# Performance work log

Measured on AMD Instinct MI355X. Metric: run time of the kernel, lower is better.

## Reference

```python
import jax, jax.numpy as jnp
import numpy as np

NUM_HEADS = 12
LOCAL_WINDOW = 7


def setup_inputs() -> dict:
    key = jax.random.key(0)
    k1, k2, k3 = jax.random.split(key, 3)
    B, N, C = 2, 2048, 768
    x = jax.random.normal(k1, (B, N, C), dtype=jnp.float32)
    w_qkv = jax.random.normal(k2, (3 * C, C), dtype=jnp.float32) * (C ** -0.5)
    w_proj = jax.random.normal(k3, (C, C), dtype=jnp.float32) * (C ** -0.5)
    b_proj = jnp.zeros((C,), dtype=jnp.float32)
    return {"x": x, "w_qkv": w_qkv, "w_proj": w_proj, "b_proj": b_proj}


def reference(x, w_qkv, w_proj, b_proj):
    B, N, C = x.shape
    H = NUM_HEADS
    Dh = C // H
    scale = Dh ** -0.5
    # local-window additive mask: 0 within |i-j|<=w, -inf outside (vectorized)
    idx = jnp.arange(N)
    local_mask = jnp.where(
        jnp.abs(idx[:, None] - idx[None, :]) <= LOCAL_WINDOW, 0.0, -jnp.inf
    ).astype(x.dtype)
    qkv = x @ w_qkv.T
    qkv = qkv.reshape(B, N, 3, H, Dh).transpose(2, 0, 3, 1, 4)
    q, k, v = qkv[0], qkv[1], qkv[2]
    attn = jnp.einsum("bhnd,bhmd->bhnm", q, k) * scale
    attn = attn + local_mask[None, None, :, :]
    attn = jax.nn.softmax(attn, axis=-1)
    out = jnp.einsum("bhnm,bhmd->bhnd", attn, v)
    out = out.transpose(0, 2, 1, 3).reshape(B, N, C)
    return out @ w_proj.T + b_proj
```

## Files before the change

### kernel.cpp

```cpp
#include <hip/hip_runtime.h>
#include <hip/hip_bf16.h>

typedef __bf16 bf16;
typedef bf16 bf16x4 __attribute__((ext_vector_type(4)));
typedef bf16 bf16x8 __attribute__((ext_vector_type(8)));
typedef float floatx4 __attribute__((ext_vector_type(4)));

#define GLOBAL_AS __attribute__((address_space(1)))
#define LDS_AS __attribute__((address_space(3)))

__global__ __launch_bounds__(256)
void cvt3_f32_bf16(const float* __restrict__ s0, const float* __restrict__ s1,
                   const float* __restrict__ s2, bf16* __restrict__ d0,
                   bf16* __restrict__ d1, bf16* __restrict__ d2,
                   int n0, int n1, int n2)
{
    int t = blockIdx.x * blockDim.x + threadIdx.x;
    const float* s; bf16* d; int i;
    if (t < n0)                { s = s0; d = d0; i = t; }
    else if (t < n0 + n1)      { s = s1; d = d1; i = t - n0; }
    else if (t < n0 + n1 + n2) { s = s2; d = d2; i = t - n0 - n1; }
    else return;
    float4 v = ((const float4*)s)[i];
    bf16x4 o = { (bf16)v.x, (bf16)v.y, (bf16)v.z, (bf16)v.w };
    ((bf16x4*)d)[i] = o;
}

template<typename CT, bool AF32, bool WF32, int TM, int M, int N, int K,
         int LDA, int LDC>
__global__ __launch_bounds__(256, 2)
void gemm_bt(const void* __restrict__ Av, const void* __restrict__ Wv,
             CT* __restrict__ C, const float* __restrict__ bias)
{
    constexpr int MI = TM / 32;
    __shared__ __align__(16) bf16 As[TM * 32];
    __shared__ __align__(16) bf16 Bs[128 * 32];

    const int tid  = threadIdx.x;
    const int lane = tid & 63;
    const int wave = tid >> 6;

    const int lin = blockIdx.y * gridDim.x + blockIdx.x;
    const int ch  = gridDim.x >> 3;
    const int xcd = lin & 7;
    const int rr  = lin >> 3;
    const int bx  = xcd * ch + (rr % ch);
    const int by  = rr / ch;

    const int row0 = bx * TM;
    const int col0 = by * 128;

    const int wm = (wave & 1) * (TM / 2);
    const int wn = (wave >> 1) * 64;

    floatx4 acc[MI][4] = {};

    const int fr = lane & 15;
    const int fk = (lane >> 4) * 8;

    const int lr = lane >> 2;
    const int lk = (lane & 3) * 8;

    for (int k0 = 0; k0 < K; k0 += 32) {
        if (AF32) {
            constexpr int NV = TM * 4;
            #pragma unroll
            for (int c = 0; c < NV / 256; ++c) {
                const int idx = tid + c * 256;
                const int r   = idx >> 2;
                const int cb  = (idx & 3) * 8;
                const float4* g = (const float4*)((const float*)Av
                                   + (size_t)(row0 + r) * LDA + k0 + cb);
                float4 g0 = g[0], g1 = g[1];
                bf16x8 va;
                va[0]=(bf16)g0.x; va[1]=(bf16)g0.y; va[2]=(bf16)g0.z; va[3]=(bf16)g0.w;
                va[4]=(bf16)g1.x; va[5]=(bf16)g1.y; va[6]=(bf16)g1.z; va[7]=(bf16)g1.w;
                *(bf16x8*)(As + r * 32 + cb) = va;
            }
        } else {
            constexpr int CAW = TM / 64;
            #pragma unroll
            for (int c = 0; c < CAW; ++c) {
                const int chunk = wave * CAW + c;
                const int r = chunk * 16 + lr;
                const bf16* gA = (const bf16*)Av + (size_t)(row0 + r) * LDA + k0 + lk;
                __builtin_amdgcn_global_load_lds((const GLOBAL_AS void*)gA,
                                                 (LDS_AS void*)(As + chunk * 512),
                                                 16, 0, 0);
            }
        }
        if (WF32) {
            #pragma unroll
            for (int c = 0; c < 2; ++c) {
                const int idx = tid + c * 256;
                const int r   = idx >> 2;
                const int cb  = (idx & 3) * 8;
                const float4* g = (const float4*)((const float*)Wv
                                   + (size_t)(col0 + r) * K + k0 + cb);
                float4 g0 = g[0], g1 = g[1];
                bf16x8 vw;
                vw[0]=(bf16)g0.x; vw[1]=(bf16)g0.y; vw[2]=(bf16)g0.z; vw[3]=(bf16)g0.w;
                vw[4]=(bf16)g1.x; vw[5]=(bf16)g1.y; vw[6]=(bf16)g1.z; vw[7]=(bf16)g1.w;
                *(bf16x8*)(Bs + r * 32 + cb) = vw;
            }
        } else {
            #pragma unroll
            for (int c = 0; c < 2; ++c) {
                const int chunk = wave * 2 + c;
                const int r = chunk * 16 + lr;
                const bf16* gB = (const bf16*)Wv + (size_t)(col0 + r) * K + k0 + lk;
                __builtin_amdgcn_global_load_lds((const GLOBAL_AS void*)gB,
                                                 (LDS_AS void*)(Bs + chunk * 512),
                                                 16, 0, 0);
            }
        }
        __syncthreads();

        bf16x8 af[MI], bfr[4];
        #pragma unroll
        for (int i = 0; i < MI; ++i)
            af[i]  = *(const bf16x8*)(As + (wm + i * 16 + fr) * 32 + fk);
        #pragma unroll
        for (int j = 0; j < 4; ++j)
            bfr[j] = *(const bf16x8*)(Bs + (wn + j * 16 + fr) * 32 + fk);
        #pragma unroll
        for (int i = 0; i < MI; ++i)
            #pragma unroll
            for (int j = 0; j < 4; ++j)
                acc[i][j] = __builtin_amdgcn_mfma_f32_16x16x32_bf16(
                    af[i], bfr[j], acc[i][j], 0, 0, 0);

        __syncthreads();
    }

    const int fc  = lane & 15;
    const int fr4 = (lane >> 4) * 4;
    #pragma unroll
    for (int i = 0; i < MI; ++i) {
        #pragma unroll
        for (int j = 0; j < 4; ++j) {
            const int col = col0 + wn + j * 16 + fc;
            const float b = bias ? bias[col] : 0.0f;
            #pragma unroll
            for (int r = 0; r < 4; ++r) {
                const int row = row0 + wm + i * 16 + fr4 + r;
                C[(size_t)row * LDC + col] = (CT)(acc[i][j][r] + b);
            }
        }
    }
}

__global__ __launch_bounds__(256)
void attn_tile(const bf16* __restrict__ qkv, bf16* __restrict__ aout)
{
    __shared__ __align__(16) bf16 Vt[4][64][40];
    __shared__ __align__(16) bf16 Ps[4][16][40];

    const int w    = threadIdx.x >> 6;
    const int lane = threadIdx.x & 63;
    const int c    = lane & 15;
    const int q    = lane >> 4;
    int bid = blockIdx.x;
    bid = (bid & 7) * 96 + (bid >> 3);
    const int wid  = bid * 4 + w;
    const int it   = wid & 127;
    const int bh   = wid >> 7;
    const int h    = bh % 12;
    const int b    = bh / 12;
    const int I0   = it * 16;
    const int bbase = b * 2048;
    const int j0   = I0 - 7;

    #pragma unroll
    for (int itr = 0; itr < 4; ++itr) {
        int idx = itr * 64 + lane;
        int row = idx >> 3;
        int dc  = (idx & 7) * 8;
        int jc  = j0 + row; jc = jc < 0 ? 0 : (jc > 2047 ? 2047 : jc);
        const bf16* base = qkv + (size_t)(bbase + jc) * 2304 + 1536 + h * 64 + dc;
        bf16x8 vv = *(const bf16x8*)base;
        #pragma unroll
        for (int e = 0; e < 8; ++e) {
            int d    = dc + e;
            int col2 = (row * 2) ^ (((d >> 3) & 3) << 4);
            *(bf16*)((char*)&Vt[w][d][0] + col2) = vv[e];
        }
    }

    const bf16* qrow = qkv + (size_t)(bbase + I0 + c) * 2304 + h * 64;
    bf16x8 aq0 = *(const bf16x8*)(qrow + q * 8);
    bf16x8 aq1 = *(const bf16x8*)(qrow + 32 + q * 8);

    floatx4 st[2] = {};
    #pragma unroll
    for (int t = 0; t < 2; ++t) {
        int jr = j0 + t * 16 + c;
        jr = jr < 0 ? 0 : (jr > 2047 ? 2047 : jr);
        const bf16* krow = qkv + (size_t)(bbase + jr) * 2304 + 768 + h * 64;
        bf16x8 k0 = *(const bf16x8*)(krow + q * 8);
        bf16x8 k1 = *(const bf16x8*)(krow + 32 + q * 8);
        st[t] = __builtin_amdgcn_mfma_f32_16x16x32_bf16(aq0, k0, st[t], 0, 0, 0);
        st[t] = __builtin_amdgcn_mfma_f32_16x16x32_bf16(aq1, k1, st[t], 0, 0, 0);
    }

    float s[2][4];
    #pragma unroll
    for (int t = 0; t < 2; ++t)
        #pragma unroll
        for (int r = 0; r < 4; ++r) {
            int il = q * 4 + r;
            int jl = t * 16 + c;
            int ja = j0 + jl;
            bool valid = (jl >= il) && (jl <= il + 14) && (ja >= 0) && (ja < 2048);
            s[t][r] = valid ? st[t][r] * 0.125f : -1e30f;
        }

    float l[4], p[2][4];
    #pragma unroll
    for (int r = 0; r < 4; ++r) {
        float m2 = fmaxf(s[0][r], s[1][r]);
        #pragma unroll
        for (int mk = 1; mk < 16; mk <<= 1) m2 = fmaxf(m2, __shfl_xor(m2, mk, 64));
        p[0][r] = __expf(s[0][r] - m2);
        p[1][r] = __expf(s[1][r] - m2);
        float l2 = p[0][r] + p[1][r];
        #pragma unroll
        for (int mk = 1; mk < 16; mk <<= 1) l2 += __shfl_xor(l2, mk, 64);
        l[r] = l2;
    }

    #pragma unroll
    for (int r = 0; r < 4; ++r) {
        Ps[w][q * 4 + r][c]      = (bf16)p[0][r];
        Ps[w][q * 4 + r][16 + c] = (bf16)p[1][r];
    }

    bf16x8 ap = *(const bf16x8*)(&Ps[w][c][q * 8]);
    floatx4 ov[4];
    #pragma unroll
    for (int nt = 0; nt < 4; ++nt) {
        int dr = nt * 16 + c;
        int cb = (q * 16) ^ (((dr >> 3) & 3) << 4);
        bf16x8 vf = *(const bf16x8*)((const char*)&Vt[w][dr][0] + cb);
        floatx4 z = {};
        ov[nt] = __builtin_amdgcn_mfma_f32_16x16x32_bf16(ap, vf, z, 0, 0, 0);
    }

    float rl[4];
    #pragma unroll
    for (int r = 0; r < 4; ++r) rl[r] = 1.0f / l[r];
    #pragma unroll
    for (int r = 0; r < 4; ++r) {
        bf16* orow = aout + (size_t)(bbase + I0 + q * 4 + r) * 768 + h * 64;
        #pragma unroll
        for (int nt = 0; nt < 4; ++nt)
            orow[nt * 16 + c] = (bf16)(ov[nt][r] * rl[r]);
    }
}

extern "C" void kernel_launch(void* const* d_in, const int* in_sizes, int n_in,
                              void* d_out, int out_size, void* d_ws, size_t ws_size,
                              hipStream_t stream)
{
    const float* x      = (const float*)d_in[0];
    const float* w_qkv  = (const float*)d_in[1];
    const float* w_proj = (const float*)d_in[2];
    const float* b_proj = (const float*)d_in[3];
    float* out = (float*)d_out;

    bf16* qkv = (bf16*)d_ws;
    const size_t QKV_B  = (size_t)4096 * 2304 * 2;
    const size_t AO_B   = (size_t)4096 * 768 * 2;
    const size_t XB_B   = (size_t)4096 * 768 * 2;
    const size_t WQKV_B = (size_t)2304 * 768 * 2;
    const size_t WPRJ_B = (size_t)768 * 768 * 2;

    if (ws_size >= QKV_B + AO_B + XB_B + WQKV_B + WPRJ_B) {
        bf16* aout = (bf16*)((char*)d_ws + QKV_B);
        bf16* xb   = (bf16*)((char*)aout + AO_B);
        bf16* wqb  = (bf16*)((char*)xb + XB_B);
        bf16* wpb  = (bf16*)((char*)wqb + WQKV_B);

        const int n0 = 4096 * 768 / 4, n1 = 2304 * 768 / 4, n2 = 768 * 768 / 4;
        cvt3_f32_bf16<<<dim3((n0 + n1 + n2) / 256), 256, 0, stream>>>(
            x, w_qkv, w_proj, xb, wqb, wpb, n0, n1, n2);

        gemm_bt<bf16, false, false, 128, 4096, 2304, 768, 768, 2304>
            <<<dim3(32, 18), 256, 0, stream>>>(xb, wqb, qkv, nullptr);

        attn_tile<<<dim3(768), 256, 0, stream>>>(qkv, aout);

        gemm_bt<float, false, false, 64, 4096, 768, 768, 768, 768>
            <<<dim3(64, 6), 256, 0, stream>>>(aout, wpb, out, b_proj);
    } else {
        gemm_bt<bf16, true, true, 128, 4096, 2304, 768, 768, 2304>
            <<<dim3(32, 18), 256, 0, stream>>>(x, w_qkv, qkv, nullptr);

        bf16* aout = (bf16*)((char*)d_ws + QKV_B);
        attn_tile<<<dim3(768), 256, 0, stream>>>(qkv, aout);

        gemm_bt<float, false, true, 64, 4096, 768, 768, 768, 768>
            <<<dim3(64, 6), 256, 0, stream>>>(aout, w_proj, out, b_proj);
    }
}
```

Measured before the change: 121.9 us.

## Use 256x256-tile 8-wave GEMM with direct-to-LDS loads for QKV projection

Adds a new GEMM kernel with 512 threads and 256x256 output tiles. It double-buffers K=64 slices loaded straight into LDS via global_load_lds with XOR swizzling, and splits MFMA work into quadrants with set-priority and barriers. It replaces the older 128-row tile GEMM for the QKV projection only. The goal is more data reuse per block and overlapping loads with compute. In exchange it launches only 144 blocks, fewer than the number of CUs, and uses 128KB of LDS, which limits occupancy.

```diff
diff --git a/kernel.cpp b/kernel.cpp
--- a/kernel.cpp
+++ b/kernel.cpp
@@ -8,6 +8,12 @@
 
 #define GLOBAL_AS __attribute__((address_space(1)))
 #define LDS_AS __attribute__((address_space(3)))
+
+__device__ __forceinline__ void hard_barrier() {
+    asm volatile("" ::: "memory");
+    __builtin_amdgcn_s_barrier();
+    asm volatile("" ::: "memory");
+}
 
 __global__ __launch_bounds__(256)
 void cvt3_f32_bf16(const float* __restrict__ s0, const float* __restrict__ s1,
@@ -26,6 +32,125 @@
     ((bf16x4*)d)[i] = o;
 }
 
+template<typename CT, int M, int N, int K, int LDA, int LDC>
+__global__ __launch_bounds__(512, 2)
+void gemm8p_bt(const bf16* __restrict__ A, const bf16* __restrict__ W,
+               CT* __restrict__ C)
+{
+    constexpr int NT = K / 64;
+    __shared__ __align__(16) bf16 lds[2][2][256 * 64];
+
+    const int tid  = threadIdx.x;
+    const int lane = tid & 63;
+    const int wave = tid >> 6;
+
+    int lin = blockIdx.x;
+    const int chx = gridDim.x >> 3;
+    lin = (lin & 7) * chx + (lin >> 3);
+    const int bx = lin / (N / 256);
+    const int by = lin % (N / 256);
+    const int row0 = bx * 256;
+    const int col0 = by * 256;
+
+    const int wm = (wave & 1) * 128;
+    const int wn = (wave >> 1) * 64;
+
+    const int fr  = lane & 15;
+    const int fks = lane >> 4;
+    const int fr7 = fr & 7;
+
+    const int rl = tid >> 3;
+    const int sl = tid & 7;
+    const int ss = sl ^ (rl & 7);
+
+    floatx4 acc[8][4] = {};
+
+    auto stage = [&](const bf16* G, int ldg, int g0, int k0, bf16* Ld) {
+        #pragma unroll
+        for (int c = 0; c < 4; ++c) {
+            const bf16* src = G + (size_t)(g0 + c * 64 + rl) * ldg + k0 + ss * 8;
+            __builtin_amdgcn_global_load_lds((const GLOBAL_AS void*)src,
+                (LDS_AS void*)(Ld + c * 4096 + wave * 512), 16, 0, 0);
+        }
+    };
+
+    bf16x8 afA[4][2], bf0[2][2], bf1[2][2];
+
+    auto loadA = [&](const bf16* Ab, int qi) {
+        #pragma unroll
+        for (int ii = 0; ii < 4; ++ii)
+            #pragma unroll
+            for (int kk = 0; kk < 2; ++kk)
+                afA[ii][kk] = *(const bf16x8*)(Ab
+                    + (wm + (qi + ii) * 16 + fr) * 64
+                    + (((kk * 4 + fks) ^ fr7) * 8));
+    };
+    auto loadB = [&](const bf16* Bb, int qj, bf16x8 (&bb)[2][2]) {
+        #pragma unroll
+        for (int jj = 0; jj < 2; ++jj)
+            #pragma unroll
+            for (int kk = 0; kk < 2; ++kk)
+                bb[jj][kk] = *(const bf16x8*)(Bb
+                    + (wn + (qj + jj) * 16 + fr) * 64
+                    + (((kk * 4 + fks) ^ fr7) * 8));
+    };
+    auto mfmaQ = [&](int qi, int qj, bf16x8 (&bb)[2][2]) {
+        __builtin_amdgcn_s_setprio(1);
+        #pragma unroll
+        for (int ii = 0; ii < 4; ++ii)
+            #pragma unroll
+            for (int jj = 0; jj < 2; ++jj)
+                #pragma unroll
+                for (int kk = 0; kk < 2; ++kk)
+                    acc[qi + ii][qj + jj] =
+                        __builtin_amdgcn_mfma_f32_16x16x32_bf16(
+                            afA[ii][kk], bb[jj][kk], acc[qi + ii][qj + jj],
+                            0, 0, 0);
+        __builtin_amdgcn_s_setprio(0);
+        hard_barrier();
+    };
+
+    stage(A, LDA, row0, 0, lds[0][0]);
+    stage(W, K,   col0, 0, lds[0][1]);
+
+    for (int t = 0; t < NT; ++t) {
+        const int buf = t & 1;
+        const bf16* Ab = lds[buf][0];
+        const bf16* Bb = lds[buf][1];
+        if (t + 1 < NT) {
+            stage(A, LDA, row0, (t + 1) * 64, lds[buf ^ 1][0]);
+            stage(W, K,   col0, (t + 1) * 64, lds[buf ^ 1][1]);
+            asm volatile("s_waitcnt vmcnt(8)" ::: "memory");
+        } else {
+            asm volatile("s_waitcnt vmcnt(0)" ::: "memory");
+        }
+        hard_barrier();
+
+        loadA(Ab, 0);
+        loadB(Bb, 0, bf0);
+        loadB(Bb, 2, bf1);
+        mfmaQ(0, 0, bf0);
+        mfmaQ(0, 2, bf1);
+        loadA(Ab, 4);
+        mfmaQ(4, 2, bf1);
+        mfmaQ(4, 0, bf0);
+    }
+
+    const int fc  = lane & 15;
+    const int fr4 = (lane >> 4) * 4;
+    #pragma unroll
+    for (int i = 0; i < 8; ++i)
+        #pragma unroll
+        for (int j = 0; j < 4; ++j) {
+            const int col = col0 + wn + j * 16 + fc;
+            #pragma unroll
+            for (int r = 0; r < 4; ++r) {
+                const int row = row0 + wm + i * 16 + fr4 + r;
+                C[(size_t)row * LDC + col] = (CT)acc[i][j][r];
+            }
+        }
+}
+
 template<typename CT, bool AF32, bool WF32, int TM, int M, int N, int K,
          int LDA, int LDC>
 __global__ __launch_bounds__(256, 2)
@@ -285,8 +410,8 @@
         cvt3_f32_bf16<<<dim3((n0 + n1 + n2) / 256), 256, 0, stream>>>(
             x, w_qkv, w_proj, xb, wqb, wpb, n0, n1, n2);
 
-        gemm_bt<bf16, false, false, 128, 4096, 2304, 768, 768, 2304>
-            <<<dim3(32, 18), 256, 0, stream>>>(xb, wqb, qkv, nullptr);
+        gemm8p_bt<bf16, 4096, 2304, 768, 768, 2304>
+            <<<dim3(144), 512, 0, stream>>>(xb, wqb, qkv);
 
         attn_tile<<<dim3(768), 256, 0, stream>>>(qkv, aout);
 
```

After: 123.5 us. No clear change (+1.3%).
